# Kernel optimization log

Measured on AMD Instinct MI355X. Metric: run time of the kernel, lower is better.

Reference implementation:

```python
import jax, jax.numpy as jnp
import numpy as np

D = 1024
E = 8


def setup_inputs() -> dict:
    key = jax.random.key(0)
    ks = jax.random.split(key, 7)
    s = 1.0 / np.sqrt(D)
    x = jax.random.normal(ks[0], (4, 2048, D), dtype=jnp.float32)
    Wg = jax.random.uniform(ks[1], (D, E), minval=-s, maxval=s, dtype=jnp.float32)
    bg = jax.random.uniform(ks[2], (E,), minval=-s, maxval=s, dtype=jnp.float32)
    W1 = jax.random.uniform(ks[3], (E, D, D), minval=-s, maxval=s, dtype=jnp.float32)
    b1 = jax.random.uniform(ks[4], (E, D), minval=-s, maxval=s, dtype=jnp.float32)
    W2 = jax.random.uniform(ks[5], (E, D, D), minval=-s, maxval=s, dtype=jnp.float32)
    b2 = jax.random.uniform(ks[6], (E, D), minval=-s, maxval=s, dtype=jnp.float32)
    return {"x": x, "Wg": Wg, "bg": bg, "W1": W1, "b1": b1, "W2": W2, "b2": b2}


def reference(x, Wg, bg, W1, b1, W2, b2):
    N, T, d = x.shape
    x_flat = x.reshape(N * T, d)                                  # [NT, D]
    logits = x_flat @ Wg + bg                                     # [NT, E]
    probs = jax.nn.softmax(logits, axis=-1)
    assignments = jnp.argmax(probs, axis=-1)                      # [NT]
    # all-experts MLP (dense, as in the original module)
    h = jnp.einsum('nd,edh->neh', x_flat, W1) + b1[None]          # [NT, E, D]
    h = jax.nn.gelu(h, approximate=False)                         # torch GELU = exact erf
    eo = jnp.einsum('neh,ehd->ned', h, W2) + b2[None]             # [NT, E, D]
    selected = jnp.take_along_axis(eo, assignments[:, None, None], axis=1)[:, 0, :]  # [NT, D]
    w = jnp.take_along_axis(probs, assignments[:, None], axis=1)  # [NT, 1]
    out = (w * selected).reshape(N, T, d)
    return out
```

## Files before the change

kernel.cpp:

```cpp
#include <hip/hip_runtime.h>
#include <cstdint>

#define NT 8192
#define DD 1024
#define NE 8
#define BK 64
#define NKIT (DD / BK)
#define MAXTILE 72

typedef __attribute__((ext_vector_type(8))) _Float16 half8;
typedef __attribute__((ext_vector_type(4))) float f32x4;

__device__ __forceinline__ unsigned short f2h_bits(float f) {
  _Float16 h = (_Float16)f;
  return __builtin_bit_cast(unsigned short, h);
}

#define GLDS16(gp, lp) __builtin_amdgcn_global_load_lds( \
  (__attribute__((address_space(1))) void*)(uintptr_t)(gp), \
  (__attribute__((address_space(3))) void*)(uintptr_t)(lp), 16, 0, 0)

__global__ __launch_bounds__(256) void wcast_kernel(
    const float* __restrict__ W1, const float* __restrict__ W2,
    _Float16* __restrict__ W1t, _Float16* __restrict__ W2t) {
  __shared__ float tile[64][65];
  const int z = blockIdx.z;
  const float* W = (z < 8 ? W1 : W2) + (size_t)(z & 7) * (DD * DD);
  _Float16* Wt   = (z < 8 ? W1t : W2t) + (size_t)(z & 7) * (DD * DD);
  const int k0 = blockIdx.x * 64, n0 = blockIdx.y * 64;
  const int tid = threadIdx.x;
#pragma unroll
  for (int it = 0; it < 4; ++it) {
    int idx = it * 256 + tid;
    int r = idx >> 4;
    int q = idx & 15;
    float4 v = *(const float4*)(W + (size_t)(k0 + r) * DD + n0 + q * 4);
    tile[r][q * 4 + 0] = v.x; tile[r][q * 4 + 1] = v.y;
    tile[r][q * 4 + 2] = v.z; tile[r][q * 4 + 3] = v.w;
  }
  __syncthreads();
#pragma unroll
  for (int it = 0; it < 4; ++it) {
    int idx = it * 256 + tid;
    int n = idx >> 4;
    int q = idx & 15;
    ushort4 o;
    o.x = f2h_bits(tile[q * 4 + 0][n]);
    o.y = f2h_bits(tile[q * 4 + 1][n]);
    o.z = f2h_bits(tile[q * 4 + 2][n]);
    o.w = f2h_bits(tile[q * 4 + 3][n]);
    *(ushort4*)(Wt + (size_t)(n0 + n) * DD + k0 + q * 4) = o;
  }
}

__global__ __launch_bounds__(256) void gate_kernel(
    const float* __restrict__ x, const float* __restrict__ Wg, const float* __restrict__ bg,
    int* __restrict__ assign, float* __restrict__ wgt, _Float16* __restrict__ xh) {
  __shared__ float WgL[NE * DD];
  const int tid = threadIdx.x;
#pragma unroll
  for (int it = 0; it < 8; ++it) {
    int idx = it * 256 + tid;
    float4 v = ((const float4*)Wg)[idx];
    int k = idx >> 1;
    int e0 = (idx & 1) * 4;
    WgL[(e0 + 0) * DD + k] = v.x;
    WgL[(e0 + 1) * DD + k] = v.y;
    WgL[(e0 + 2) * DD + k] = v.z;
    WgL[(e0 + 3) * DD + k] = v.w;
  }
  __syncthreads();
  const int lane = tid & 63, w = tid >> 6;
#pragma unroll
  for (int s = 0; s < 2; ++s) {
    const int t = blockIdx.x * 8 + w * 2 + s;
    const float4* xr = (const float4*)(x + (size_t)t * DD);
    float4 xv[4];
#pragma unroll
    for (int c = 0; c < 4; ++c) xv[c] = xr[lane + 64 * c];
    ushort4* xo = (ushort4*)(xh + (size_t)t * DD);
#pragma unroll
    for (int c = 0; c < 4; ++c) {
      union { ushort4 u; _Float16 h[4]; } cv;
      cv.h[0] = (_Float16)xv[c].x; cv.h[1] = (_Float16)xv[c].y;
      cv.h[2] = (_Float16)xv[c].z; cv.h[3] = (_Float16)xv[c].w;
      xo[lane + 64 * c] = cv.u;
    }
    float p[NE];
#pragma unroll
    for (int e = 0; e < NE; ++e) {
      float acc = 0.f;
#pragma unroll
      for (int c = 0; c < 4; ++c) {
        float4 wv = *(const float4*)&WgL[e * DD + 4 * lane + 256 * c];
        acc += xv[c].x * wv.x + xv[c].y * wv.y + xv[c].z * wv.z + xv[c].w * wv.w;
      }
      p[e] = acc;
    }
#pragma unroll
    for (int e = 0; e < NE; ++e) {
      float v = p[e];
      for (int off = 32; off > 0; off >>= 1) v += __shfl_down(v, off, 64);
      p[e] = v;
    }
    if (lane == 0) {
      float l[NE];
#pragma unroll
      for (int e = 0; e < NE; ++e) l[e] = p[e] + bg[e];
      int a = 0; float best = l[0];
#pragma unroll
      for (int e = 1; e < NE; ++e) if (l[e] > best) { best = l[e]; a = e; }
      float sum = 0.f;
#pragma unroll
      for (int e = 0; e < NE; ++e) sum += expf(l[e] - best);
      assign[t] = a;
      wgt[t] = 1.0f / sum;
    }
  }
}

__global__ __launch_bounds__(1024) void sort_kernel(
    const int* __restrict__ assign, int* __restrict__ rowtok, int* __restrict__ plan) {
  __shared__ int sc[NE * 1024];
  const int tid = threadIdx.x;
  int a[8];
  int c[NE];
#pragma unroll
  for (int e = 0; e < NE; ++e) c[e] = 0;
#pragma unroll
  for (int j = 0; j < 8; ++j) { a[j] = assign[tid * 8 + j]; ++c[a[j]]; }
#pragma unroll
  for (int e = 0; e < NE; ++e) sc[e * 1024 + tid] = c[e];
  __syncthreads();
  for (int d = 1; d < 1024; d <<= 1) {
    int add[NE];
    if (tid >= d) {
#pragma unroll
      for (int e = 0; e < NE; ++e) add[e] = sc[e * 1024 + tid - d];
    }
    __syncthreads();
    if (tid >= d) {
#pragma unroll
      for (int e = 0; e < NE; ++e) sc[e * 1024 + tid] += add[e];
    }
    __syncthreads();
  }
  int tot[NE], incl[NE];
#pragma unroll
  for (int e = 0; e < NE; ++e) { tot[e] = sc[e * 1024 + 1023]; incl[e] = sc[e * 1024 + tid]; }
  int offs[NE];
  {
    int s = 0;
#pragma unroll
    for (int e = 0; e < NE; ++e) { offs[e] = s; s += tot[e]; }
  }
  int run[NE];
#pragma unroll
  for (int e = 0; e < NE; ++e) run[e] = offs[e] + incl[e] - c[e];
#pragma unroll
  for (int j = 0; j < 8; ++j) { int e = a[j]; rowtok[run[e]++] = tid * 8 + j; }
  if (tid == 0) {
    int nt = 0;
    for (int e = 0; e < NE; ++e) {
      int cc = tot[e], st = offs[e];
      int t_cnt = (cc + 127) >> 7;
      for (int t = 0; t < t_cnt; ++t) {
        plan[1 + nt] = e;
        plan[1 + MAXTILE + nt] = st + t * 128;
        plan[1 + 2 * MAXTILE + nt] = st + cc;
        ++nt;
      }
    }
    plan[0] = nt;
  }
}

template <int MODE>
__global__ __launch_bounds__(256) void gemm_kernel(
    const _Float16* __restrict__ A,
    const _Float16* __restrict__ Wt,
    const float* __restrict__ bias,
    const int* __restrict__ plan,
    _Float16* __restrict__ Hout,
    float* __restrict__ Fout,
    const int* __restrict__ rowtok,
    const float* __restrict__ wgt) {
  const int wrk = blockIdx.x;
  const int tile = wrk >> 3;
  if (tile >= plan[0]) return;
  const int e = plan[1 + tile];
  const int m0 = plan[1 + MAXTILE + tile];
  const int seg_end = plan[1 + 2 * MAXTILE + tile];
  const int n0 = (wrk & 7) * 128;

  const int tid = threadIdx.x;
  const int lane = tid & 63;
  const int w = tid >> 6;
  const int wm = w >> 1, wn = w & 1;
  const int quad = lane >> 4;
  const int r15 = lane & 15;

  __shared__ alignas(16) _Float16 As[2 * 128 * BK];
  __shared__ alignas(16) _Float16 Bs[2 * 128 * BK];

  const _Float16* We = Wt + (size_t)e * DD * DD;
  const _Float16* gAp[4];
  const _Float16* gBp[4];
  int ldso[4];
#pragma unroll
  for (int i = 0; i < 4; ++i) {
    int slot = i * 256 + tid;
    int row = slot >> 3;
    int c = (slot & 7) ^ (row & 7);
    int rg = m0 + row; if (rg > NT - 1) rg = NT - 1;
    int arow = (MODE == 0) ? rowtok[rg] : rg;
    gAp[i] = A + (size_t)arow * DD + c * 8;
    gBp[i] = We + (size_t)(n0 + row) * DD + c * 8;
    ldso[i] = slot * 16;
  }

  int aoff[2][4], boff[2][4];
#pragma unroll
  for (int ks = 0; ks < 2; ++ks)
#pragma unroll
    for (int i = 0; i < 4; ++i) {
      int m = wm * 64 + i * 16 + r15;
      aoff[ks][i] = m * 8 + ((ks * 4 + quad) ^ (m & 7));
      int n = wn * 64 + i * 16 + r15;
      boff[ks][i] = n * 8 + ((ks * 4 + quad) ^ (n & 7));
    }

  f32x4 acc[4][4];
  f32x4 zero4 = {0.f, 0.f, 0.f, 0.f};
#pragma unroll
  for (int mi = 0; mi < 4; ++mi)
#pragma unroll
    for (int ni = 0; ni < 4; ++ni) acc[mi][ni] = zero4;

  char* ldsA = (char*)As;
  char* ldsB = (char*)Bs;

#define STAGE(K0, BUF) do {                                          \
    char* la_ = ldsA + ((BUF) << 14);                                \
    char* lb_ = ldsB + ((BUF) << 14);                                \
    _Pragma("unroll") for (int i_ = 0; i_ < 4; ++i_)                 \
      GLDS16(gAp[i_] + (K0), la_ + ldso[i_]);                        \
    _Pragma("unroll") for (int i_ = 0; i_ < 4; ++i_)                 \
      GLDS16(gBp[i_] + (K0), lb_ + ldso[i_]);                        \
  } while (0)

  STAGE(0, 0);

#pragma unroll 1
  for (int kt = 0; kt < NKIT; ++kt) {
    const int buf = kt & 1;
    __syncthreads();
    if (kt + 1 < NKIT) STAGE((kt + 1) * BK, buf ^ 1);
    const half8* AsV = (const half8*)(ldsA + (buf << 14));
    const half8* BsV = (const half8*)(ldsB + (buf << 14));
#pragma unroll
    for (int ks = 0; ks < 2; ++ks) {
      half8 a[4], b[4];
#pragma unroll
      for (int i = 0; i < 4; ++i) a[i] = AsV[aoff[ks][i]];
#pragma unroll
      for (int i = 0; i < 4; ++i) b[i] = BsV[boff[ks][i]];
#pragma unroll
      for (int mi = 0; mi < 4; ++mi)
#pragma unroll
        for (int ni = 0; ni < 4; ++ni)
          acc[mi][ni] = __builtin_amdgcn_mfma_f32_16x16x32_f16(a[mi], b[ni], acc[mi][ni], 0, 0, 0);
    }
  }
#undef STAGE

  const float* bptr = bias + (size_t)e * DD;
  if (MODE == 0) {
#pragma unroll
    for (int mi = 0; mi < 4; ++mi) {
      int rowb = m0 + wm * 64 + mi * 16 + quad * 4;
#pragma unroll
      for (int r = 0; r < 4; ++r) {
        int gpos = rowb + r;
        if (gpos < seg_end) {
#pragma unroll
          for (int ni = 0; ni < 4; ++ni) {
            int n = n0 + wn * 64 + ni * 16 + r15;
            float val = acc[mi][ni][r] + bptr[n];
            val = 0.5f * val * (1.0f + erff(val * 0.70710678118654752f));
            Hout[(size_t)gpos * DD + n] = (_Float16)val;
          }
        }
      }
    }
  } else {
#pragma unroll
    for (int mi = 0; mi < 4; ++mi) {
      int rowb = m0 + wm * 64 + mi * 16 + quad * 4;
#pragma unroll
      for (int r = 0; r < 4; ++r) {
        int gpos = rowb + r;
        if (gpos < seg_end) {
          int tok = rowtok[gpos];
          float wv = wgt[tok];
          float* orow = Fout + (size_t)tok * DD;
#pragma unroll
          for (int ni = 0; ni < 4; ++ni) {
            int n = n0 + wn * 64 + ni * 16 + r15;
            orow[n] = (acc[mi][ni][r] + bptr[n]) * wv;
          }
        }
      }
    }
  }
}

extern "C" void kernel_launch(void* const* d_in, const int* in_sizes, int n_in,
                              void* d_out, int out_size, void* d_ws, size_t ws_size,
                              hipStream_t stream) {
  const float* x  = (const float*)d_in[0];
  const float* Wg = (const float*)d_in[1];
  const float* bg = (const float*)d_in[2];
  const float* W1 = (const float*)d_in[3];
  const float* b1 = (const float*)d_in[4];
  const float* W2 = (const float*)d_in[5];
  const float* b2 = (const float*)d_in[6];
  float* out = (float*)d_out;

  char* ws = (char*)d_ws;
  const size_t MB16 = (size_t)1 << 24;
  _Float16* W1t = (_Float16*)(ws + 0 * MB16);
  _Float16* W2t = (_Float16*)(ws + 1 * MB16);
  _Float16* xh  = (_Float16*)(ws + 2 * MB16);
  _Float16* H   = (_Float16*)(ws + 3 * MB16);
  int*   assign = (int*)(ws + 4 * MB16);
  int*   rowtok = assign + NT;
  float* wgt    = (float*)(rowtok + NT);
  int*   plan   = (int*)(wgt + NT);

  wcast_kernel<<<dim3(16, 16, 16), 256, 0, stream>>>(W1, W2, W1t, W2t);
  gate_kernel<<<NT / 8, 256, 0, stream>>>(x, Wg, bg, assign, wgt, xh);
  sort_kernel<<<1, 1024, 0, stream>>>(assign, rowtok, plan);
  gemm_kernel<0><<<MAXTILE * 8, 256, 0, stream>>>(xh, W1t, b1, plan, H, nullptr, rowtok, nullptr);
  gemm_kernel<1><<<MAXTILE * 8, 256, 0, stream>>>(H, W2t, b2, plan, nullptr, out, rowtok, wgt);
}
```

Baseline: 259.2 us.

## Switch GEMM to four-stage LDS pipeline with BK=32 and explicit vmcnt waits

Halves the K tile to 32 and keeps four LDS buffers instead of two, prefetching three tiles ahead with direct global-to-LDS loads. The generic __syncthreads is replaced by s_barrier plus explicit vmcnt waits, so each iteration waits only for its own tile while later tiles stay in flight. The LDS swizzle and fragment offsets are reworked for 64-byte rows. The aim is to hide global load latency better. In exchange there are two barriers per iteration and half as many MFMAs between them, which adds synchronisation overhead.

```diff
diff --git a/kernel.cpp b/kernel.cpp
--- a/kernel.cpp
+++ b/kernel.cpp
@@ -4,7 +4,7 @@
 #define NT 8192
 #define DD 1024
 #define NE 8
-#define BK 64
+#define BK 32
 #define NKIT (DD / BK)
 #define MAXTILE 72
 
@@ -19,6 +19,11 @@
 #define GLDS16(gp, lp) __builtin_amdgcn_global_load_lds( \
   (__attribute__((address_space(1))) void*)(uintptr_t)(gp), \
   (__attribute__((address_space(3))) void*)(uintptr_t)(lp), 16, 0, 0)
+
+#define WAITCNT_VM12 0xF7C
+#define WAITCNT_VM8  0xF78
+#define WAITCNT_VM4  0xF74
+#define WAITCNT_VM0  0xF70
 
 __global__ __launch_bounds__(256) void wcast_kernel(
     const float* __restrict__ W1, const float* __restrict__ W2,
@@ -200,18 +205,20 @@
   const int quad = lane >> 4;
   const int r15 = lane & 15;
 
-  __shared__ alignas(16) _Float16 As[2 * 128 * BK];
-  __shared__ alignas(16) _Float16 Bs[2 * 128 * BK];
+  __shared__ alignas(16) _Float16 As[4 * 128 * BK];
+  __shared__ alignas(16) _Float16 Bs[4 * 128 * BK];
+  char* ldsA = (char*)As;
+  char* ldsB = (char*)Bs;
 
   const _Float16* We = Wt + (size_t)e * DD * DD;
-  const _Float16* gAp[4];
-  const _Float16* gBp[4];
-  int ldso[4];
-#pragma unroll
-  for (int i = 0; i < 4; ++i) {
+  const _Float16* gAp[2];
+  const _Float16* gBp[2];
+  int ldso[2];
+#pragma unroll
+  for (int i = 0; i < 2; ++i) {
     int slot = i * 256 + tid;
-    int row = slot >> 3;
-    int c = (slot & 7) ^ (row & 7);
+    int row = slot >> 2;
+    int c = (slot & 3) ^ ((row >> 1) & 3);
     int rg = m0 + row; if (rg > NT - 1) rg = NT - 1;
     int arow = (MODE == 0) ? rowtok[rg] : rg;
     gAp[i] = A + (size_t)arow * DD + c * 8;
@@ -219,16 +226,14 @@
     ldso[i] = slot * 16;
   }
 
-  int aoff[2][4], boff[2][4];
-#pragma unroll
-  for (int ks = 0; ks < 2; ++ks)
-#pragma unroll
-    for (int i = 0; i < 4; ++i) {
-      int m = wm * 64 + i * 16 + r15;
-      aoff[ks][i] = m * 8 + ((ks * 4 + quad) ^ (m & 7));
-      int n = wn * 64 + i * 16 + r15;
-      boff[ks][i] = n * 8 + ((ks * 4 + quad) ^ (n & 7));
-    }
+  int aoff[4], boff[4];
+#pragma unroll
+  for (int i = 0; i < 4; ++i) {
+    int m = wm * 64 + i * 16 + r15;
+    aoff[i] = m * 4 + (quad ^ ((m >> 1) & 3));
+    int n = wn * 64 + i * 16 + r15;
+    boff[i] = n * 4 + (quad ^ ((n >> 1) & 3));
+  }
 
   f32x4 acc[4][4];
   f32x4 zero4 = {0.f, 0.f, 0.f, 0.f};
@@ -237,40 +242,43 @@
 #pragma unroll
     for (int ni = 0; ni < 4; ++ni) acc[mi][ni] = zero4;
 
-  char* ldsA = (char*)As;
-  char* ldsB = (char*)Bs;
-
-#define STAGE(K0, BUF) do {                                          \
-    char* la_ = ldsA + ((BUF) << 14);                                \
-    char* lb_ = ldsB + ((BUF) << 14);                                \
-    _Pragma("unroll") for (int i_ = 0; i_ < 4; ++i_)                 \
-      GLDS16(gAp[i_] + (K0), la_ + ldso[i_]);                        \
-    _Pragma("unroll") for (int i_ = 0; i_ < 4; ++i_)                 \
-      GLDS16(gBp[i_] + (K0), lb_ + ldso[i_]);                        \
+#define STAGE(KT) do {                                               \
+    const int b_ = (KT) & 3;                                         \
+    char* la_ = ldsA + (b_ << 13);                                   \
+    char* lb_ = ldsB + (b_ << 13);                                   \
+    const int ko_ = (KT) * BK;                                       \
+    _Pragma("unroll") for (int i_ = 0; i_ < 2; ++i_)                 \
+      GLDS16(gAp[i_] + ko_, la_ + ldso[i_]);                         \
+    _Pragma("unroll") for (int i_ = 0; i_ < 2; ++i_)                 \
+      GLDS16(gBp[i_] + ko_, lb_ + ldso[i_]);                         \
   } while (0)
 
-  STAGE(0, 0);
+  STAGE(0); STAGE(1); STAGE(2);
 
 #pragma unroll 1
   for (int kt = 0; kt < NKIT; ++kt) {
-    const int buf = kt & 1;
-    __syncthreads();
-    if (kt + 1 < NKIT) STAGE((kt + 1) * BK, buf ^ 1);
-    const half8* AsV = (const half8*)(ldsA + (buf << 14));
-    const half8* BsV = (const half8*)(ldsB + (buf << 14));
-#pragma unroll
-    for (int ks = 0; ks < 2; ++ks) {
-      half8 a[4], b[4];
-#pragma unroll
-      for (int i = 0; i < 4; ++i) a[i] = AsV[aoff[ks][i]];
-#pragma unroll
-      for (int i = 0; i < 4; ++i) b[i] = BsV[boff[ks][i]];
-#pragma unroll
-      for (int mi = 0; mi < 4; ++mi)
-#pragma unroll
-        for (int ni = 0; ni < 4; ++ni)
-          acc[mi][ni] = __builtin_amdgcn_mfma_f32_16x16x32_f16(a[mi], b[ni], acc[mi][ni], 0, 0, 0);
-    }
+    __builtin_amdgcn_s_barrier();
+    __asm__ volatile("" ::: "memory");
+    if (kt + 3 < NKIT) STAGE(kt + 3);
+    if (kt < NKIT - 3)      __builtin_amdgcn_s_waitcnt(WAITCNT_VM12);
+    else if (kt == NKIT - 3) __builtin_amdgcn_s_waitcnt(WAITCNT_VM8);
+    else if (kt == NKIT - 2) __builtin_amdgcn_s_waitcnt(WAITCNT_VM4);
+    else                     __builtin_amdgcn_s_waitcnt(WAITCNT_VM0);
+    __builtin_amdgcn_s_barrier();
+    __asm__ volatile("" ::: "memory");
+    const int buf = kt & 3;
+    const half8* AsV = (const half8*)(ldsA + (buf << 13));
+    const half8* BsV = (const half8*)(ldsB + (buf << 13));
+    half8 a[4], b[4];
+#pragma unroll
+    for (int i = 0; i < 4; ++i) a[i] = AsV[aoff[i]];
+#pragma unroll
+    for (int i = 0; i < 4; ++i) b[i] = BsV[boff[i]];
+#pragma unroll
+    for (int mi = 0; mi < 4; ++mi)
+#pragma unroll
+      for (int ni = 0; ni < 4; ++ni)
+        acc[mi][ni] = __builtin_amdgcn_mfma_f32_16x16x32_f16(a[mi], b[ni], acc[mi][ni], 0, 0, 0);
   }
 #undef STAGE
 
```

New measurement: 262.5 us. About the same (+1.3%).
